# Kernel tuning notes

Measured on AMD Instinct MI355X. Metric: run time of the kernel, lower is better.

## Reference

```python
import jax, jax.numpy as jnp
from jax import lax
import numpy as np

B, T, H, W = 2, 16, 128, 128
HID = 256
EPS = 1e-5


def _conv(x, w):
    # x: (N,C,H,W), w: (O,I,3,3), stride 1, pad 1 ('SAME')
    return lax.conv_general_dilated(x, w, (1, 1), 'SAME',
                                    dimension_numbers=('NCHW', 'OIHW', 'NCHW'))


def _cnn_block(x, w, b, g, be, m, v):
    # conv -> BatchNorm (eval mode) -> ReLU -> MaxPool2d(2)
    y = _conv(x, w) + b[None, :, None, None]
    scale = (g * lax.rsqrt(v + EPS))[None, :, None, None]
    shift = (be - m * g * lax.rsqrt(v + EPS))[None, :, None, None]
    y = jax.nn.relu(y * scale + shift)
    return lax.reduce_window(y, -jnp.inf, lax.max,
                             (1, 1, 2, 2), (1, 1, 2, 2), 'VALID')


def _convlstm_layer(xs, Wg, bg):
    # xs: (T,B,Cin,h,w); gate conv on concat([x,h]) -> 4*HID channels
    _, nB, _, h, w = xs.shape
    h0 = jnp.zeros((nB, HID, h, w), xs.dtype)

    def step(carry, x_t):
        hprev, cprev = carry
        z = _conv(jnp.concatenate([x_t, hprev], axis=1), Wg) + bg[None, :, None, None]
        ci, cf, co, cg = jnp.split(z, 4, axis=1)
        c = jax.nn.sigmoid(cf) * cprev + jax.nn.sigmoid(ci) * jnp.tanh(cg)
        hn = jax.nn.sigmoid(co) * jnp.tanh(c)
        return (hn, c), hn

    (_, _), hs = lax.scan(step, (h0, h0), xs)
    return hs  # (T,B,HID,h,w)


def setup_inputs() -> dict:
    key = jax.random.key(0)
    ks = jax.random.split(key, 12)

    def rn(k, shape, s=0.05):
        return jax.random.normal(k, shape, jnp.float32) * s

    inp = {'x': jax.random.normal(ks[0], (B, T, 1, H, W), jnp.float32)}
    chans = [(1, 64), (64, 128), (128, 256)]
    for i, (ci, co) in enumerate(chans):
        inp[f'w{i}'] = rn(ks[1 + i], (co, ci, 3, 3))
        inp[f'b{i}'] = jnp.zeros((co,), jnp.float32)
        inp[f'g{i}'] = jnp.ones((co,), jnp.float32)
        inp[f'be{i}'] = jnp.zeros((co,), jnp.float32)
        inp[f'm{i}'] = rn(ks[4 + i], (co,), 0.01)
        inp[f'v{i}'] = jnp.ones((co,), jnp.float32)
    for l in range(2):
        cin = 256 if l == 0 else HID
        inp[f'lw{l}'] = rn(ks[7 + l], (4 * HID, cin + HID, 3, 3))
        inp[f'lb{l}'] = jnp.zeros((4 * HID,), jnp.float32)
    return inp


def reference(x, w0, b0, g0, be0, m0, v0,
              w1, b1, g1, be1, m1, v1,
              w2, b2, g2, be2, m2, v2,
              lw0, lb0, lw1, lb1):
    nB, nT = x.shape[0], x.shape[1]
    y = x.reshape(nB * nT, x.shape[2], x.shape[3], x.shape[4])
    y = _cnn_block(y, w0, b0, g0, be0, m0, v0)   # (BT,64,64,64)
    y = _cnn_block(y, w1, b1, g1, be1, m1, v1)   # (BT,128,32,32)
    y = _cnn_block(y, w2, b2, g2, be2, m2, v2)   # (BT,256,16,16)
    y = y.reshape(nB, nT, y.shape[1], y.shape[2], y.shape[3])
    xs = jnp.transpose(y, (1, 0, 2, 3, 4))       # (T,B,256,16,16)
    hs = _convlstm_layer(xs, lw0, lb0)
    hs = _convlstm_layer(hs, lw1, lb1)
    z_seq = jnp.transpose(hs, (1, 0, 2, 3, 4))   # (B,T,HID,16,16)
    z_last = z_seq[:, -1]
    return (z_seq, z_last)
```

## Files before the change

### kernel.cpp

```cpp
#include <hip/hip_runtime.h>
#include <hip/hip_bf16.h>
#include <cstddef>
#include <cstdint>

#define BN_EPS 1e-5f

typedef __attribute__((ext_vector_type(8))) _Float16 half8;
typedef __attribute__((ext_vector_type(4))) _Float16 half4;
typedef __attribute__((ext_vector_type(4))) float f32x4;

#define GLOBAL_AS __attribute__((address_space(1)))
#define LDS_AS    __attribute__((address_space(3)))

__device__ __forceinline__ void gload_lds16(const void* g, void* l) {
    __builtin_amdgcn_global_load_lds((const GLOBAL_AS uint32_t*)g,
                                     (LDS_AS uint32_t*)l, 16, 0, 0);
}

__device__ __forceinline__ float sigmoidf_(float x) {
    return 1.f / (1.f + __expf(-x));
}
__device__ __forceinline__ float tanhf_(float x) {
    float e = __expf(2.f * x);
    return 1.f - 2.f / (e + 1.f);
}

template <int CI, int OC, int S, int OCB>
__global__ __launch_bounds__(256) void cnn_block1_kernel(
    const float* __restrict__ in, const float* __restrict__ w,
    const float* __restrict__ bias, const float* __restrict__ g,
    const float* __restrict__ be, const float* __restrict__ m,
    const float* __restrict__ v, _Float16* __restrict__ out)
{
    constexpr int PS  = S / 2;
    constexpr int NQ  = (PS * PS) / 256;
    constexpr int NOG = OC / OCB;
    __shared__ float wl[OCB * CI * 9];

    int bid  = blockIdx.x;
    int quad = bid % NQ;
    int t2   = bid / NQ;
    int ocg  = t2 % NOG;
    int img  = t2 / NOG;
    int tid  = threadIdx.x;
    int oc0  = ocg * OCB;

    const float* wsrc = w + (size_t)oc0 * CI * 9;
    for (int i = tid; i < OCB * CI * 9; i += 256) wl[i] = wsrc[i];
    __syncthreads();

    int pp = quad * 256 + tid;
    int pr = pp / PS, pc = pp % PS;
    int r0 = 2 * pr - 1, c0 = 2 * pc - 1;

    int  roff[4], coff[4];
    bool rok[4], cok[4];
#pragma unroll
    for (int i = 0; i < 4; i++) {
        int rr = r0 + i; rok[i] = (rr >= 0 && rr < S); roff[i] = min(max(rr, 0), S - 1) * S;
        int cc = c0 + i; cok[i] = (cc >= 0 && cc < S); coff[i] = min(max(cc, 0), S - 1);
    }

    float acc[OCB][4];
#pragma unroll
    for (int o = 0; o < OCB; o++)
#pragma unroll
        for (int j = 0; j < 4; j++) acc[o][j] = 0.f;

    const float* ip = in + (size_t)img * CI * S * S;
    for (int ci = 0; ci < CI; ++ci) {
        float patch[4][4];
#pragma unroll
        for (int iy = 0; iy < 4; iy++)
#pragma unroll
            for (int ix = 0; ix < 4; ix++) {
                float val = ip[roff[iy] + coff[ix]];
                patch[iy][ix] = (rok[iy] && cok[ix]) ? val : 0.f;
            }
#pragma unroll
        for (int o = 0; o < OCB; o++) {
            const float* wp = wl + ((size_t)o * CI + ci) * 9;
#pragma unroll
            for (int ky = 0; ky < 3; ky++)
#pragma unroll
                for (int kx = 0; kx < 3; kx++) {
                    float ww = wp[ky * 3 + kx];
                    acc[o][0] += ww * patch[ky][kx];
                    acc[o][1] += ww * patch[ky][kx + 1];
                    acc[o][2] += ww * patch[ky + 1][kx];
                    acc[o][3] += ww * patch[ky + 1][kx + 1];
                }
        }
        ip += S * S;
    }

    half8 hv;
#pragma unroll
    for (int o = 0; o < OCB; o++) {
        int oc = oc0 + o;
        float scale = g[oc] * rsqrtf(v[oc] + BN_EPS);
        float shift = be[oc] - m[oc] * scale + bias[oc] * scale;
        float r00 = fmaxf(acc[o][0] * scale + shift, 0.f);
        float r01 = fmaxf(acc[o][1] * scale + shift, 0.f);
        float r10 = fmaxf(acc[o][2] * scale + shift, 0.f);
        float r11 = fmaxf(acc[o][3] * scale + shift, 0.f);
        hv[o] = (_Float16)fmaxf(fmaxf(r00, r01), fmaxf(r10, r11));
    }
    *(half8*)(&out[((size_t)img * (PS * PS) + pp) * OC + oc0]) = hv;
}

template <int OC, int CI>
__global__ __launch_bounds__(256) void wprep_conv_kernel(
    const float* __restrict__ W, _Float16* __restrict__ Wc)
{
    constexpr int K  = CI * 9;
    constexpr int CH = K / 8;
    int idx = blockIdx.x * 256 + threadIdx.x;
    if (idx >= OC * CH) return;
    int oc = idx / CH, chunk = idx % CH;
    int k0   = chunk * 8;
    int kcp  = (k0 >> 3) & 3;
    int kcl  = kcp ^ ((oc >> 1) & 3);
    int klog = (k0 & ~31) | (kcl << 3);
    int tap = klog / CI, ci = klog % CI;
    const float* src = W + ((size_t)oc * CI + ci) * 9 + tap;
    _Float16* dst = Wc + (size_t)oc * K + k0;
#pragma unroll
    for (int j = 0; j < 8; ++j) dst[j] = (_Float16)src[(size_t)j * 9];
}

__global__ __launch_bounds__(256) void wprep_kernel(
    const float* __restrict__ W, _Float16* __restrict__ Wp)
{
    int idx   = blockIdx.x * 256 + threadIdx.x;
    int row   = idx / 576;
    int chunk = idx % 576;
    int k0    = chunk * 8;
    int kcell = k0 >> 5;
    int kcp   = (k0 >> 3) & 3;
    int kcl   = kcp ^ ((row >> 1) & 3);
    int klog  = kcell * 32 + kcl * 8;
    int c = row >> 2, ggate = row & 3;
    int zc = ggate * 256 + c;
    int part = (klog >= 2304) ? 1 : 0;
    int rem  = klog - part * 2304;
    int tap  = rem >> 8;
    int ci   = rem & 255;
    const float* src = W + (size_t)zc * 4608 + (size_t)(part * 256 + ci) * 9 + tap;
    _Float16* dst = Wp + (size_t)row * 4608 + k0;
#pragma unroll
    for (int j = 0; j < 8; ++j) dst[j] = (_Float16)src[(size_t)j * 9];
}

template <int CI, int OC, int SIN>
__global__ __launch_bounds__(256) void conv_mfma_kernel(
    const _Float16* __restrict__ Wc, const _Float16* __restrict__ in,
    const float* __restrict__ bias, const float* __restrict__ g,
    const float* __restrict__ be, const float* __restrict__ m,
    const float* __restrict__ v, const _Float16* __restrict__ zpage,
    _Float16* __restrict__ out)
{
    constexpr int K    = CI * 9;
    constexpr int KS   = K / 32;
    constexpr int SPT  = CI / 32;
    constexpr int NPX  = SIN * SIN;
    constexpr int POOL = SIN / 2;
    constexpr int NPP  = NPX / 4;
    constexpr int NT     = (32 * NPX) / 64;
    constexpr int NCHUNK = NT / 8;

    __shared__ _Float16 Al[2][4096];
    __shared__ _Float16 Bl[2][2048];

    const int tid = threadIdx.x;
    const int gx   = blockIdx.x & 7;
    const int rest = blockIdx.x >> 3;
    const int nb   = gx * NCHUNK + (rest % NCHUNK);
    const int bm   = rest / NCHUNK;

    const int n0  = nb * 64;
    const int img = n0 / NPX;
    const int r   = n0 - img * NPX;

    const int srow = tid >> 2;
    const int kc   = tid & 3;
    const int kcs  = kc ^ ((srow >> 1) & 3);
    const int wid  = tid >> 6;

    const _Float16* aptr  = Wc + (size_t)(bm * 128 + srow) * K + kc * 8;
    const _Float16* aptr2 = aptr + (size_t)64 * K;

    const int rn   = r + srow;
    const int ppix = rn >> 2, quad = rn & 3;
    const int y = (ppix / POOL) * 2 + (quad >> 1);
    const int x = (ppix % POOL) * 2 + (quad & 1);
    const _Float16* imgbase = in + (size_t)img * NPX * CI;

    const int lane = tid & 63;
    const int kq   = lane >> 4;
    const int acol = lane & 15;
    int a_off[2], b_off[4];
#pragma unroll
    for (int mf = 0; mf < 2; mf++) {
        int arow = wid * 32 + mf * 16 + acol;
        a_off[mf] = arow * 64 + ((kq ^ ((arow >> 1) & 3)) << 4);
    }
#pragma unroll
    for (int nf = 0; nf < 4; nf++) {
        int brow = nf * 16 + acol;
        b_off[nf] = brow * 64 + ((kq ^ ((brow >> 1) & 3)) << 4);
    }

    f32x4 acc[2][4];
#pragma unroll
    for (int mf = 0; mf < 2; mf++)
#pragma unroll
        for (int nf = 0; nf < 4; nf++) acc[mf][nf] = {0.f, 0.f, 0.f, 0.f};

    auto stage = [&](int s, int buf) {
        gload_lds16(aptr  + (size_t)s * 32, (char*)&Al[buf][0] + wid * 1024);
        gload_lds16(aptr2 + (size_t)s * 32, (char*)&Al[buf][0] + 4096 + wid * 1024);
        int tap = s / SPT;
        int ci0 = (s % SPT) * 32;
        int dy = tap / 3 - 1, dx = tap - (tap / 3) * 3 - 1;
        int yy = y + dy, xx = x + dx;
        bool ok = (yy >= 0) && (yy < SIN) && (xx >= 0) && (xx < SIN);
        const _Float16* base = ok ? (imgbase + (size_t)(yy * SIN + xx) * CI) : zpage;
        gload_lds16(base + ci0 + kcs * 8, (char*)&Bl[buf][0] + wid * 1024);
    };

    stage(0, 0);
    __syncthreads();

    for (int s = 0; s < KS; ++s) {
        int cur = s & 1;
        if (s + 1 < KS) stage(s + 1, cur ^ 1);

        half8 af[2], bf[4];
#pragma unroll
        for (int mf = 0; mf < 2; mf++)
            af[mf] = *(const half8*)((const char*)&Al[cur][0] + a_off[mf]);
#pragma unroll
        for (int nf = 0; nf < 4; nf++)
            bf[nf] = *(const half8*)((const char*)&Bl[cur][0] + b_off[nf]);
#pragma unroll
        for (int mf = 0; mf < 2; mf++)
#pragma unroll
            for (int nf = 0; nf < 4; nf++)
                acc[mf][nf] = __builtin_amdgcn_mfma_f32_16x16x32_f16(
                    af[mf], bf[nf], acc[mf][nf], 0, 0, 0);

        __syncthreads();
    }

#pragma unroll
    for (int mf = 0; mf < 2; mf++) {
        const int oc0w = bm * 128 + wid * 32 + mf * 16 + kq * 4;
        float sc[4], sh[4];
#pragma unroll
        for (int j = 0; j < 4; j++) {
            int oc = oc0w + j;
            sc[j] = g[oc] * rsqrtf(v[oc] + BN_EPS);
            sh[j] = be[oc] - m[oc] * sc[j] + bias[oc] * sc[j];
        }
#pragma unroll
        for (int nf = 0; nf < 4; nf++) {
            f32x4 a = acc[mf][nf];
            half4 hv;
#pragma unroll
            for (int j = 0; j < 4; j++) {
                float val = fmaxf(a[j] * sc[j] + sh[j], 0.f);
                val = fmaxf(val, __shfl_xor(val, 1));
                val = fmaxf(val, __shfl_xor(val, 2));
                hv[j] = (_Float16)val;
            }
            if ((acol & 3) == 0) {
                int pl = (r + nf * 16 + acol) >> 2;
                *(half4*)(&out[((size_t)img * NPP + pl) * OC + oc0w]) = hv;
            }
        }
    }
}

struct Seg {
    const _Float16* W;
    const float* lbias;
    const _Float16* hsrc; long hs;
    _Float16* zx;  long zxs;
    float* cstate;
    _Float16* hdst; long hds;
    float* outseq; long osb;
    float* outlast;
    int mode;
};

__global__ __launch_bounds__(256, 4) void lstm3_kernel(
    Seg s0, Seg s1, Seg s2, Seg s3, int e0, int e1, int e2,
    const _Float16* __restrict__ zpage)
{
    __shared__ _Float16 Al[6][2048];
    __shared__ _Float16 Bl[6][1024];

    const int b = blockIdx.x;
    Seg S; int i;
    if (b < e0)      { S = s0; i = b; }
    else if (b < e1) { S = s1; i = b - e0; }
    else if (b < e2) { S = s2; i = b - e1; }
    else             { S = s3; i = b - e2; }

    const int tid = threadIdx.x;
    const int bm  = (i & 7) | (((i >> 3) & 1) << 3);
    const int nn  = i >> 4;
    const int img = nn >> 3;
    const int px0 = (nn & 7) * 32;

    const int wid  = tid >> 6;
    const int lane = tid & 63;
    const int lrow = lane >> 2;
    const int kc   = lane & 3;
    const int rowt = wid * 16 + lrow;
    const int kcs  = kc ^ ((rowt >> 1) & 3);

    const _Float16* aptr = S.W + (size_t)(bm * 64 + rowt) * 4608 + kc * 8;

    const int p_pix = px0 + rowt;
    const int py = p_pix >> 4, px = p_pix & 15;

    const _Float16* srcH = S.hsrc + (size_t)img * S.hs;

    const int kq   = lane >> 4;
    const int acol = lane & 15;
    const int arow = wid * 16 + acol;
    const int a_off  = arow * 64 + ((kq ^ ((arow >> 1) & 3)) << 4);
    const int b_off0 = acol * 64 + ((kq ^ ((acol >> 1) & 3)) << 4);
    const int brow1  = 16 + acol;
    const int b_off1 = brow1 * 64 + ((kq ^ ((brow1 >> 1) & 3)) << 4);

    f32x4 acc0 = {0.f, 0.f, 0.f, 0.f};
    f32x4 acc1 = {0.f, 0.f, 0.f, 0.f};

    const int NPAIR = 36;

    auto stage_pair = [&](int sp, int b2) {
        gload_lds16(aptr + (size_t)sp * 32,       (char*)&Al[b2][0]     + wid * 1024);
        gload_lds16(aptr + (size_t)(sp + 1) * 32, (char*)&Al[b2 + 1][0] + wid * 1024);
        if (wid < 2) {
            int tap = sp >> 3;
            int cc  = sp & 7;
            int t3  = tap / 3;
            int dy = t3 - 1, dx = tap - t3 * 3 - 1;
            int yy = py + dy, xx = px + dx;
            bool ok = (yy >= 0) && (yy < 16) && (xx >= 0) && (xx < 16);
            const _Float16* bsrc = ok ? (srcH + (size_t)(yy * 16 + xx) * 256) : zpage;
            const _Float16* p0 = bsrc + cc * 32 + kcs * 8;
            gload_lds16(p0,      (char*)&Bl[b2][0]     + wid * 1024);
            gload_lds16(p0 + 32, (char*)&Bl[b2 + 1][0] + wid * 1024);
        }
    };

    stage_pair(0, 0);
    stage_pair(2, 2);

    int cb = 0;
    int ib = 4;
    for (int p = 0; p < NPAIR; ++p) {
        __builtin_amdgcn_sched_barrier(0);
        if (wid < 2) {
            if (p < NPAIR - 1) asm volatile("s_waitcnt vmcnt(4)" ::: "memory");
            else               asm volatile("s_waitcnt vmcnt(0)" ::: "memory");
        } else {
            if (p < NPAIR - 1) asm volatile("s_waitcnt vmcnt(2)" ::: "memory");
            else               asm volatile("s_waitcnt vmcnt(0)" ::: "memory");
        }
        __builtin_amdgcn_s_barrier();
        int sp = 2 * p + 4;
        if (sp < 72) stage_pair(sp, ib);

        {
            half8 af  = *(const half8*)((const char*)&Al[cb][0] + a_off);
            half8 bf0 = *(const half8*)((const char*)&Bl[cb][0] + b_off0);
            half8 bf1 = *(const half8*)((const char*)&Bl[cb][0] + b_off1);
            acc0 = __builtin_amdgcn_mfma_f32_16x16x32_f16(af, bf0, acc0, 0, 0, 0);
            acc1 = __builtin_amdgcn_mfma_f32_16x16x32_f16(af, bf1, acc1, 0, 0, 0);
        }
        {
            half8 af  = *(const half8*)((const char*)&Al[cb + 1][0] + a_off);
            half8 bf0 = *(const half8*)((const char*)&Bl[cb + 1][0] + b_off0);
            half8 bf1 = *(const half8*)((const char*)&Bl[cb + 1][0] + b_off1);
            acc0 = __builtin_amdgcn_mfma_f32_16x16x32_f16(af, bf0, acc0, 0, 0, 0);
            acc1 = __builtin_amdgcn_mfma_f32_16x16x32_f16(af, bf1, acc1, 0, 0, 0);
        }

        cb = (cb == 4) ? 0 : cb + 2;
        ib = (ib == 4) ? 0 : ib + 2;
    }

    const int c = bm * 16 + wid * 4 + kq;

    if (S.mode == 1) {
#pragma unroll
        for (int cN = 0; cN < 2; ++cN) {
            f32x4 a = cN ? acc1 : acc0;
            int pxg = px0 + cN * 16 + acol;
            half4 hv;
#pragma unroll
            for (int j = 0; j < 4; j++) hv[j] = (_Float16)a[j];
            *(half4*)(&S.zx[(size_t)img * S.zxs + ((size_t)c * 256 + pxg) * 4]) = hv;
        }
        return;
    }

    float bi  = S.lbias[c];
    float bf_ = S.lbias[256 + c];
    float bo  = S.lbias[512 + c];
    float bg  = S.lbias[768 + c];

#pragma unroll
    for (int cN = 0; cN < 2; ++cN) {
        f32x4 a = cN ? acc1 : acc0;
        int pxg = px0 + cN * 16 + acol;
        half4 zv = *(const half4*)(&S.zx[(size_t)img * S.zxs + ((size_t)c * 256 + pxg) * 4]);
        size_t off = (size_t)img * 65536 + (size_t)c * 256 + pxg;
        float zi = a[0] + (float)zv[0] + bi;
        float zf = a[1] + (float)zv[1] + bf_;
        float zo = a[2] + (float)zv[2] + bo;
        float zg = a[3] + (float)zv[3] + bg;
        float cold = S.cstate[off];
        float cn = sigmoidf_(zf) * cold + sigmoidf_(zi) * tanhf_(zg);
        float hn = sigmoidf_(zo) * tanhf_(cn);
        S.cstate[off] = cn;
        S.hdst[(size_t)img * S.hds + (size_t)pxg * 256 + c] = (_Float16)hn;
        if (S.outseq) {
            S.outseq[(size_t)img * S.osb + (size_t)c * 256 + pxg] = hn;
            if (S.outlast)
                S.outlast[(size_t)img * 65536 + (size_t)c * 256 + pxg] = hn;
        }
    }
}

extern "C" void kernel_launch(void* const* d_in, const int* in_sizes, int n_in,
                              void* d_out, int out_size, void* d_ws, size_t ws_size,
                              hipStream_t stream)
{
    const float* x   = (const float*)d_in[0];
    const float* w0  = (const float*)d_in[1];
    const float* b0  = (const float*)d_in[2];
    const float* g0  = (const float*)d_in[3];
    const float* be0 = (const float*)d_in[4];
    const float* m0  = (const float*)d_in[5];
    const float* v0  = (const float*)d_in[6];
    const float* w1  = (const float*)d_in[7];
    const float* b1  = (const float*)d_in[8];
    const float* g1  = (const float*)d_in[9];
    const float* be1 = (const float*)d_in[10];
    const float* m1  = (const float*)d_in[11];
    const float* v1  = (const float*)d_in[12];
    const float* w2  = (const float*)d_in[13];
    const float* b2  = (const float*)d_in[14];
    const float* g2  = (const float*)d_in[15];
    const float* be2 = (const float*)d_in[16];
    const float* m2  = (const float*)d_in[17];
    const float* v2  = (const float*)d_in[18];
    const float* lw0 = (const float*)d_in[19];
    const float* lb0 = (const float*)d_in[20];
    const float* lw1 = (const float*)d_in[21];
    const float* lb1 = (const float*)d_in[22];

    float* out = (float*)d_out;

    char* base = (char*)d_ws;
    _Float16* Wp0  = (_Float16*)(base);
    _Float16* Wp1  = (_Float16*)(base + 9437184);
    _Float16* h0s  = (_Float16*)(base + 18874368);
    _Float16* y2h  = (_Float16*)(base + 25165824);
    _Float16* Wc2  = (_Float16*)(base + 29360128);
    _Float16* Wc3  = (_Float16*)(base + 29507584);
    _Float16* zpg  = (_Float16*)(base + 30097408);
    _Float16* hb1a = (_Float16*)(base + 30228480);
    _Float16* hb1b = (_Float16*)(base + 30490624);
    float*    cst0 = (float*)(base + 30752768);
    float*    cst1 = (float*)(base + 31277056);
    _Float16* zx1a = (_Float16*)(base + 31801344);
    _Float16* zx1b = (_Float16*)(base + 32849920);
    _Float16* zx0  = (_Float16*)(base + 33898496);
    _Float16* y0   = (_Float16*)(base);
    _Float16* y1   = (_Float16*)(base + 16777216);

    hipMemsetAsync(zpg, 0, 131072, stream);

    cnn_block1_kernel<1, 64, 128, 8><<<32 * 8 * 16, 256, 0, stream>>>(
        x, w0, b0, g0, be0, m0, v0, y0);
    wprep_conv_kernel<128, 64><<<36, 256, 0, stream>>>(w1, Wc2);
    conv_mfma_kernel<64, 128, 64><<<2048, 256, 0, stream>>>(
        Wc2, y0, b1, g1, be1, m1, v1, zpg, y1);
    wprep_conv_kernel<256, 128><<<144, 256, 0, stream>>>(w2, Wc3);
    conv_mfma_kernel<128, 256, 32><<<1024, 256, 0, stream>>>(
        Wc3, y1, b2, g2, be2, m2, v2, zpg, y2h);

    wprep_kernel<<<2304, 256, 0, stream>>>(lw0, Wp0);
    wprep_kernel<<<2304, 256, 0, stream>>>(lw1, Wp1);

    hipMemsetAsync(cst0, 0, (size_t)2 * 524288, stream);

    const long IS = 16 * 65536;

    auto makeD = [&](int t) {
        Seg D{};
        D.W = Wp0; D.lbias = lb0;
        D.hsrc = y2h + (size_t)t * 65536; D.hs = IS;
        D.zx = zx0 + (size_t)t * 262144; D.zxs = 16 * 262144;
        D.cstate = nullptr; D.hdst = nullptr; D.hds = 0;
        D.outseq = nullptr; D.osb = 0; D.outlast = nullptr; D.mode = 1;
        return D;
    };

    {
        Seg D0 = makeD(0), D1 = makeD(1);
        lstm3_kernel<<<512, 256, 0, stream>>>(D0, D1, D1, D1, 256, 512, 512, zpg);
    }

    for (int d = 0; d <= 17; ++d) {
        const bool doA = (d <= 15);
        const bool doC = (d >= 1 && d <= 16);
        const bool doB = (d >= 2);
        const bool doD = (d <= 13);

        Seg segs[4]; int ns = 0; int cum = 0; int ends[4];
        if (doA) {
            int t = d;
            Seg A{};
            A.W = Wp0 + 2304; A.lbias = lb0;
            A.hsrc = (t == 0) ? zpg : (h0s + (size_t)(t - 1) * 65536);
            A.hs   = (t == 0) ? 0 : IS;
            A.zx = zx0 + (size_t)t * 262144; A.zxs = 16 * 262144;
            A.cstate = cst0;
            A.hdst = h0s + (size_t)t * 65536; A.hds = IS;
            A.outseq = nullptr; A.osb = 0; A.outlast = nullptr; A.mode = 0;
            segs[ns] = A; cum += 256; ends[ns++] = cum;
        }
        if (doC) {
            int u = d - 1;
            Seg C{};
            C.W = Wp1; C.lbias = lb1;
            C.hsrc = h0s + (size_t)u * 65536; C.hs = IS;
            C.zx = (u & 1) ? zx1b : zx1a; C.zxs = 262144;
            C.cstate = nullptr; C.hdst = nullptr; C.hds = 0;
            C.outseq = nullptr; C.osb = 0; C.outlast = nullptr; C.mode = 1;
            segs[ns] = C; cum += 256; ends[ns++] = cum;
        }
        if (doB) {
            int v = d - 2;
            Seg B{};
            B.W = Wp1 + 2304; B.lbias = lb1;
            B.hsrc = (v == 0) ? zpg : ((v & 1) ? hb1a : hb1b);
            B.hs   = (v == 0) ? 0 : 65536;
            B.zx = (v & 1) ? zx1b : zx1a; B.zxs = 262144;
            B.cstate = cst1;
            B.hdst = (v & 1) ? hb1b : hb1a; B.hds = 65536;
            B.outseq = out + (size_t)v * 65536; B.osb = 1048576;
            B.outlast = (v == 15) ? (out + 2097152) : nullptr; B.mode = 0;
            segs[ns] = B; cum += 256; ends[ns++] = cum;
        }
        if (doD) {
            segs[ns] = makeD(d + 2); cum += 256; ends[ns++] = cum;
        }
        for (int k = ns; k < 4; ++k) segs[k] = segs[0];
        int e0 = ends[0];
        int e1 = (ns > 1) ? ends[1] : cum;
        int e2 = (ns > 2) ? ends[2] : cum;
        lstm3_kernel<<<cum, 256, 0, stream>>>(
            segs[0], segs[1], segs[2], segs[3], e0, e1, e2, zpg);
    }
}
```

Measured before the change: 572.8 us.

## Deepen conv pipeline to triple-buffered pairs and widen LSTM pixel tiles

The CNN conv kernel moves from a double-buffered single-step K loop with full __syncthreads to a triple-buffered pair-staged pipeline with explicit vmcnt waits, prefetching two K-steps ahead. The ConvLSTM kernel doubles its pixel tile from 32 to 64 per block, so each A-tile load feeds four MFMAs instead of two and all waves stage B. This halves the grid size per segment. The goal is better latency hiding and weight reuse, at the cost of more LDS per block and lower occupancy (launch bounds 2), plus fewer blocks in flight for the latency-bound recurrent steps.

```diff
diff --git a/kernel.cpp b/kernel.cpp
--- a/kernel.cpp
+++ b/kernel.cpp
@@ -153,7 +153,7 @@
 }
 
 template <int CI, int OC, int SIN>
-__global__ __launch_bounds__(256) void conv_mfma_kernel(
+__global__ __launch_bounds__(256, 2) void conv_mfma_kernel(
     const _Float16* __restrict__ Wc, const _Float16* __restrict__ in,
     const float* __restrict__ bias, const float* __restrict__ g,
     const float* __restrict__ be, const float* __restrict__ m,
@@ -162,6 +162,7 @@
 {
     constexpr int K    = CI * 9;
     constexpr int KS   = K / 32;
+    constexpr int NP   = KS / 2;
     constexpr int SPT  = CI / 32;
     constexpr int NPX  = SIN * SIN;
     constexpr int POOL = SIN / 2;
@@ -169,8 +170,8 @@
     constexpr int NT     = (32 * NPX) / 64;
     constexpr int NCHUNK = NT / 8;
 
-    __shared__ _Float16 Al[2][4096];
-    __shared__ _Float16 Bl[2][2048];
+    __shared__ _Float16 Al[6][4096];
+    __shared__ _Float16 Bl[6][2048];
 
     const int tid = threadIdx.x;
     const int gx   = blockIdx.x & 7;
@@ -217,40 +218,54 @@
 #pragma unroll
         for (int nf = 0; nf < 4; nf++) acc[mf][nf] = {0.f, 0.f, 0.f, 0.f};
 
-    auto stage = [&](int s, int buf) {
-        gload_lds16(aptr  + (size_t)s * 32, (char*)&Al[buf][0] + wid * 1024);
-        gload_lds16(aptr2 + (size_t)s * 32, (char*)&Al[buf][0] + 4096 + wid * 1024);
-        int tap = s / SPT;
-        int ci0 = (s % SPT) * 32;
+    auto stage_pair = [&](int sp, int b2) {
+        gload_lds16(aptr  + (size_t)sp * 32,       (char*)&Al[b2][0]            + wid * 1024);
+        gload_lds16(aptr  + (size_t)(sp + 1) * 32, (char*)&Al[b2 + 1][0]        + wid * 1024);
+        gload_lds16(aptr2 + (size_t)sp * 32,       (char*)&Al[b2][0]     + 4096 + wid * 1024);
+        gload_lds16(aptr2 + (size_t)(sp + 1) * 32, (char*)&Al[b2 + 1][0] + 4096 + wid * 1024);
+        int tap = sp / SPT;
+        int ci0 = (sp % SPT) * 32;
         int dy = tap / 3 - 1, dx = tap - (tap / 3) * 3 - 1;
         int yy = y + dy, xx = x + dx;
         bool ok = (yy >= 0) && (yy < SIN) && (xx >= 0) && (xx < SIN);
         const _Float16* base = ok ? (imgbase + (size_t)(yy * SIN + xx) * CI) : zpage;
-        gload_lds16(base + ci0 + kcs * 8, (char*)&Bl[buf][0] + wid * 1024);
+        const _Float16* p0 = base + ci0 + kcs * 8;
+        gload_lds16(p0,      (char*)&Bl[b2][0]     + wid * 1024);
+        gload_lds16(p0 + 32, (char*)&Bl[b2 + 1][0] + wid * 1024);
     };
 
-    stage(0, 0);
-    __syncthreads();
-
-    for (int s = 0; s < KS; ++s) {
-        int cur = s & 1;
-        if (s + 1 < KS) stage(s + 1, cur ^ 1);
-
-        half8 af[2], bf[4];
-#pragma unroll
-        for (int mf = 0; mf < 2; mf++)
-            af[mf] = *(const half8*)((const char*)&Al[cur][0] + a_off[mf]);
-#pragma unroll
-        for (int nf = 0; nf < 4; nf++)
-            bf[nf] = *(const half8*)((const char*)&Bl[cur][0] + b_off[nf]);
-#pragma unroll
-        for (int mf = 0; mf < 2; mf++)
+    stage_pair(0, 0);
+    stage_pair(2, 2);
+
+    int cb = 0, ib = 4;
+    for (int p = 0; p < NP; ++p) {
+        __builtin_amdgcn_sched_barrier(0);
+        if (p < NP - 1) asm volatile("s_waitcnt vmcnt(6)" ::: "memory");
+        else            asm volatile("s_waitcnt vmcnt(0)" ::: "memory");
+        __builtin_amdgcn_s_barrier();
+        int sp = 2 * p + 4;
+        if (sp < KS) stage_pair(sp, ib);
+
+#pragma unroll
+        for (int hs = 0; hs < 2; ++hs) {
+            const int bb = cb + hs;
+            half8 af[2], bf[4];
+#pragma unroll
+            for (int mf = 0; mf < 2; mf++)
+                af[mf] = *(const half8*)((const char*)&Al[bb][0] + a_off[mf]);
 #pragma unroll
             for (int nf = 0; nf < 4; nf++)
-                acc[mf][nf] = __builtin_amdgcn_mfma_f32_16x16x32_f16(
-                    af[mf], bf[nf], acc[mf][nf], 0, 0, 0);
-
-        __syncthreads();
+                bf[nf] = *(const half8*)((const char*)&Bl[bb][0] + b_off[nf]);
+#pragma unroll
+            for (int mf = 0; mf < 2; mf++)
+#pragma unroll
+                for (int nf = 0; nf < 4; nf++)
+                    acc[mf][nf] = __builtin_amdgcn_mfma_f32_16x16x32_f16(
+                        af[mf], bf[nf], acc[mf][nf], 0, 0, 0);
+        }
+
+        cb = (cb == 4) ? 0 : cb + 2;
+        ib = (ib == 4) ? 0 : ib + 2;
     }
 
 #pragma unroll
@@ -294,12 +309,12 @@
     int mode;
 };
 
-__global__ __launch_bounds__(256, 4) void lstm3_kernel(
+__global__ __launch_bounds__(256, 2) void lstm3_kernel(
     Seg s0, Seg s1, Seg s2, Seg s3, int e0, int e1, int e2,
     const _Float16* __restrict__ zpage)
 {
     __shared__ _Float16 Al[6][2048];
-    __shared__ _Float16 Bl[6][1024];
+    __shared__ _Float16 Bl[6][2048];
 
     const int b = blockIdx.x;
     Seg S; int i;
@@ -310,9 +325,9 @@
 
     const int tid = threadIdx.x;
     const int bm  = (i & 7) | (((i >> 3) & 1) << 3);
-    const int nn  = i >> 4;
-    const int img = nn >> 3;
-    const int px0 = (nn & 7) * 32;
+    const int nb  = i >> 4;
+    const int img = nb >> 2;
+    const int px0 = (nb & 3) * 64;
 
     const int wid  = tid >> 6;
     const int lane = tid & 63;
@@ -331,64 +346,56 @@
     const int kq   = lane >> 4;
     const int acol = lane & 15;
     const int arow = wid * 16 + acol;
-    const int a_off  = arow * 64 + ((kq ^ ((arow >> 1) & 3)) << 4);
-    const int b_off0 = acol * 64 + ((kq ^ ((acol >> 1) & 3)) << 4);
-    const int brow1  = 16 + acol;
-    const int b_off1 = brow1 * 64 + ((kq ^ ((brow1 >> 1) & 3)) << 4);
-
-    f32x4 acc0 = {0.f, 0.f, 0.f, 0.f};
-    f32x4 acc1 = {0.f, 0.f, 0.f, 0.f};
+    const int a_off = arow * 64 + ((kq ^ ((arow >> 1) & 3)) << 4);
+    int b_off[4];
+#pragma unroll
+    for (int nf = 0; nf < 4; nf++) {
+        int brow = nf * 16 + acol;
+        b_off[nf] = brow * 64 + ((kq ^ ((brow >> 1) & 3)) << 4);
+    }
+
+    f32x4 acc[4];
+#pragma unroll
+    for (int nf = 0; nf < 4; nf++) acc[nf] = {0.f, 0.f, 0.f, 0.f};
 
     const int NPAIR = 36;
 
     auto stage_pair = [&](int sp, int b2) {
         gload_lds16(aptr + (size_t)sp * 32,       (char*)&Al[b2][0]     + wid * 1024);
         gload_lds16(aptr + (size_t)(sp + 1) * 32, (char*)&Al[b2 + 1][0] + wid * 1024);
-        if (wid < 2) {
-            int tap = sp >> 3;
-            int cc  = sp & 7;
-            int t3  = tap / 3;
-            int dy = t3 - 1, dx = tap - t3 * 3 - 1;
-            int yy = py + dy, xx = px + dx;
-            bool ok = (yy >= 0) && (yy < 16) && (xx >= 0) && (xx < 16);
-            const _Float16* bsrc = ok ? (srcH + (size_t)(yy * 16 + xx) * 256) : zpage;
-            const _Float16* p0 = bsrc + cc * 32 + kcs * 8;
-            gload_lds16(p0,      (char*)&Bl[b2][0]     + wid * 1024);
-            gload_lds16(p0 + 32, (char*)&Bl[b2 + 1][0] + wid * 1024);
-        }
+        int tap = sp >> 3;
+        int cc  = sp & 7;
+        int t3  = tap / 3;
+        int dy = t3 - 1, dx = tap - t3 * 3 - 1;
+        int yy = py + dy, xx = px + dx;
+        bool ok = (yy >= 0) && (yy < 16) && (xx >= 0) && (xx < 16);
+        const _Float16* bsrc = ok ? (srcH + (size_t)(yy * 16 + xx) * 256) : zpage;
+        const _Float16* p0 = bsrc + cc * 32 + kcs * 8;
+        gload_lds16(p0,      (char*)&Bl[b2][0]     + wid * 1024);
+        gload_lds16(p0 + 32, (char*)&Bl[b2 + 1][0] + wid * 1024);
     };
 
     stage_pair(0, 0);
     stage_pair(2, 2);
 
-    int cb = 0;
-    int ib = 4;
+    int cb = 0, ib = 4;
     for (int p = 0; p < NPAIR; ++p) {
         __builtin_amdgcn_sched_barrier(0);
-        if (wid < 2) {
-            if (p < NPAIR - 1) asm volatile("s_waitcnt vmcnt(4)" ::: "memory");
-            else               asm volatile("s_waitcnt vmcnt(0)" ::: "memory");
-        } else {
-            if (p < NPAIR - 1) asm volatile("s_waitcnt vmcnt(2)" ::: "memory");
-            else               asm volatile("s_waitcnt vmcnt(0)" ::: "memory");
-        }
+        if (p < NPAIR - 1) asm volatile("s_waitcnt vmcnt(4)" ::: "memory");
+        else               asm volatile("s_waitcnt vmcnt(0)" ::: "memory");
         __builtin_amdgcn_s_barrier();
         int sp = 2 * p + 4;
         if (sp < 72) stage_pair(sp, ib);
 
-        {
-            half8 af  = *(const half8*)((const char*)&Al[cb][0] + a_off);
-            half8 bf0 = *(const half8*)((const char*)&Bl[cb][0] + b_off0);
-            half8 bf1 = *(const half8*)((const char*)&Bl[cb][0] + b_off1);
-            acc0 = __builtin_amdgcn_mfma_f32_16x16x32_f16(af, bf0, acc0, 0, 0, 0);
-            acc1 = __builtin_amdgcn_mfma_f32_16x16x32_f16(af, bf1, acc1, 0, 0, 0);
-        }
-        {
-            half8 af  = *(const half8*)((const char*)&Al[cb + 1][0] + a_off);
-            half8 bf0 = *(const half8*)((const char*)&Bl[cb + 1][0] + b_off0);
-            half8 bf1 = *(const half8*)((const char*)&Bl[cb + 1][0] + b_off1);
-            acc0 = __builtin_amdgcn_mfma_f32_16x16x32_f16(af, bf0, acc0, 0, 0, 0);
-            acc1 = __builtin_amdgcn_mfma_f32_16x16x32_f16(af, bf1, acc1, 0, 0, 0);
+#pragma unroll
+        for (int hs = 0; hs < 2; ++hs) {
+            const int bb = cb + hs;
+            half8 af = *(const half8*)((const char*)&Al[bb][0] + a_off);
+#pragma unroll
+            for (int nf = 0; nf < 4; nf++) {
+                half8 bf = *(const half8*)((const char*)&Bl[bb][0] + b_off[nf]);
+                acc[nf] = __builtin_amdgcn_mfma_f32_16x16x32_f16(af, bf, acc[nf], 0, 0, 0);
+            }
         }
 
         cb = (cb == 4) ? 0 : cb + 2;
@@ -399,9 +406,9 @@
 
     if (S.mode == 1) {
 #pragma unroll
-        for (int cN = 0; cN < 2; ++cN) {
-            f32x4 a = cN ? acc1 : acc0;
-            int pxg = px0 + cN * 16 + acol;
+        for (int nf = 0; nf < 4; nf++) {
+            f32x4 a = acc[nf];
+            int pxg = px0 + nf * 16 + acol;
             half4 hv;
 #pragma unroll
             for (int j = 0; j < 4; j++) hv[j] = (_Float16)a[j];
@@ -416,9 +423,9 @@
     float bg  = S.lbias[768 + c];
 
 #pragma unroll
-    for (int cN = 0; cN < 2; ++cN) {
-        f32x4 a = cN ? acc1 : acc0;
-        int pxg = px0 + cN * 16 + acol;
+    for (int nf = 0; nf < 4; nf++) {
+        f32x4 a = acc[nf];
+        int pxg = px0 + nf * 16 + acol;
         half4 zv = *(const half4*)(&S.zx[(size_t)img * S.zxs + ((size_t)c * 256 + pxg) * 4]);
         size_t off = (size_t)img * 65536 + (size_t)c * 256 + pxg;
         float zi = a[0] + (float)zv[0] + bi;
@@ -516,7 +523,7 @@
 
     {
         Seg D0 = makeD(0), D1 = makeD(1);
-        lstm3_kernel<<<512, 256, 0, stream>>>(D0, D1, D1, D1, 256, 512, 512, zpg);
+        lstm3_kernel<<<256, 256, 0, stream>>>(D0, D1, D1, D1, 128, 256, 256, zpg);
     }
 
     for (int d = 0; d <= 17; ++d) {
@@ -536,7 +543,7 @@
             A.cstate = cst0;
             A.hdst = h0s + (size_t)t * 65536; A.hds = IS;
             A.outseq = nullptr; A.osb = 0; A.outlast = nullptr; A.mode = 0;
-            segs[ns] = A; cum += 256; ends[ns++] = cum;
+            segs[ns] = A; cum += 128; ends[ns++] = cum;
         }
         if (doC) {
             int u = d - 1;
@@ -546,7 +553,7 @@
             C.zx = (u & 1) ? zx1b : zx1a; C.zxs = 262144;
             C.cstate = nullptr; C.hdst = nullptr; C.hds = 0;
             C.outseq = nullptr; C.osb = 0; C.outlast = nullptr; C.mode = 1;
-            segs[ns] = C; cum += 256; ends[ns++] = cum;
+            segs[ns] = C; cum += 128; ends[ns++] = cum;
         }
         if (doB) {
             int v = d - 2;
@@ -559,10 +566,10 @@
             B.hdst = (v & 1) ? hb1b : hb1a; B.hds = 65536;
             B.outseq = out + (size_t)v * 65536; B.osb = 1048576;
             B.outlast = (v == 15) ? (out + 2097152) : nullptr; B.mode = 0;
-            segs[ns] = B; cum += 256; ends[ns++] = cum;
+            segs[ns] = B; cum += 128; ends[ns++] = cum;
         }
         if (doD) {
-            segs[ns] = makeD(d + 2); cum += 256; ends[ns++] = cum;
+            segs[ns] = makeD(d + 2); cum += 128; ends[ns++] = cum;
         }
         for (int k = ns; k < 4; ++k) segs[k] = segs[0];
         int e0 = ends[0];
```

Measured after the change: 618.8 us. +8.0%, slower.

## Deepen conv MFMA pipeline to triple-buffered pairs of K-steps with vmcnt waits

Applied to the files above, without the earlier changes.

Replaces the double-buffered one-K-step-per-iteration loop in the CNN conv kernel with a 6-slot LDS ring that loads two K-steps per stage and keeps two pairs in flight. It waits with explicit s_waitcnt vmcnt counts and one barrier per pair, which halves the barriers and hides more global-load latency. It also adds a launch_bounds occupancy hint of 2. LDS use triples to 72KB per block, which may limit occupancy. The code assumes KS is even and large enough for the prologue.

```diff
diff --git a/kernel.cpp b/kernel.cpp
--- a/kernel.cpp
+++ b/kernel.cpp
@@ -153,7 +153,7 @@
 }
 
 template <int CI, int OC, int SIN>
-__global__ __launch_bounds__(256) void conv_mfma_kernel(
+__global__ __launch_bounds__(256, 2) void conv_mfma_kernel(
     const _Float16* __restrict__ Wc, const _Float16* __restrict__ in,
     const float* __restrict__ bias, const float* __restrict__ g,
     const float* __restrict__ be, const float* __restrict__ m,
@@ -162,6 +162,7 @@
 {
     constexpr int K    = CI * 9;
     constexpr int KS   = K / 32;
+    constexpr int NP   = KS / 2;
     constexpr int SPT  = CI / 32;
     constexpr int NPX  = SIN * SIN;
     constexpr int POOL = SIN / 2;
@@ -169,8 +170,8 @@
     constexpr int NT     = (32 * NPX) / 64;
     constexpr int NCHUNK = NT / 8;
 
-    __shared__ _Float16 Al[2][4096];
-    __shared__ _Float16 Bl[2][2048];
+    __shared__ _Float16 Al[6][4096];
+    __shared__ _Float16 Bl[6][2048];
 
     const int tid = threadIdx.x;
     const int gx   = blockIdx.x & 7;
@@ -217,40 +218,54 @@
 #pragma unroll
         for (int nf = 0; nf < 4; nf++) acc[mf][nf] = {0.f, 0.f, 0.f, 0.f};
 
-    auto stage = [&](int s, int buf) {
-        gload_lds16(aptr  + (size_t)s * 32, (char*)&Al[buf][0] + wid * 1024);
-        gload_lds16(aptr2 + (size_t)s * 32, (char*)&Al[buf][0] + 4096 + wid * 1024);
-        int tap = s / SPT;
-        int ci0 = (s % SPT) * 32;
+    auto stage_pair = [&](int sp, int b2) {
+        gload_lds16(aptr  + (size_t)sp * 32,       (char*)&Al[b2][0]            + wid * 1024);
+        gload_lds16(aptr  + (size_t)(sp + 1) * 32, (char*)&Al[b2 + 1][0]        + wid * 1024);
+        gload_lds16(aptr2 + (size_t)sp * 32,       (char*)&Al[b2][0]     + 4096 + wid * 1024);
+        gload_lds16(aptr2 + (size_t)(sp + 1) * 32, (char*)&Al[b2 + 1][0] + 4096 + wid * 1024);
+        int tap = sp / SPT;
+        int ci0 = (sp % SPT) * 32;
         int dy = tap / 3 - 1, dx = tap - (tap / 3) * 3 - 1;
         int yy = y + dy, xx = x + dx;
         bool ok = (yy >= 0) && (yy < SIN) && (xx >= 0) && (xx < SIN);
         const _Float16* base = ok ? (imgbase + (size_t)(yy * SIN + xx) * CI) : zpage;
-        gload_lds16(base + ci0 + kcs * 8, (char*)&Bl[buf][0] + wid * 1024);
+        const _Float16* p0 = base + ci0 + kcs * 8;
+        gload_lds16(p0,      (char*)&Bl[b2][0]     + wid * 1024);
+        gload_lds16(p0 + 32, (char*)&Bl[b2 + 1][0] + wid * 1024);
     };
 
-    stage(0, 0);
-    __syncthreads();
-
-    for (int s = 0; s < KS; ++s) {
-        int cur = s & 1;
-        if (s + 1 < KS) stage(s + 1, cur ^ 1);
-
-        half8 af[2], bf[4];
-#pragma unroll
-        for (int mf = 0; mf < 2; mf++)
-            af[mf] = *(const half8*)((const char*)&Al[cur][0] + a_off[mf]);
-#pragma unroll
-        for (int nf = 0; nf < 4; nf++)
-            bf[nf] = *(const half8*)((const char*)&Bl[cur][0] + b_off[nf]);
-#pragma unroll
-        for (int mf = 0; mf < 2; mf++)
+    stage_pair(0, 0);
+    stage_pair(2, 2);
+
+    int cb = 0, ib = 4;
+    for (int p = 0; p < NP; ++p) {
+        __builtin_amdgcn_sched_barrier(0);
+        if (p < NP - 1) asm volatile("s_waitcnt vmcnt(6)" ::: "memory");
+        else            asm volatile("s_waitcnt vmcnt(0)" ::: "memory");
+        __builtin_amdgcn_s_barrier();
+        int sp = 2 * p + 4;
+        if (sp < KS) stage_pair(sp, ib);
+
+#pragma unroll
+        for (int hs = 0; hs < 2; ++hs) {
+            const int bb = cb + hs;
+            half8 af[2], bf[4];
+#pragma unroll
+            for (int mf = 0; mf < 2; mf++)
+                af[mf] = *(const half8*)((const char*)&Al[bb][0] + a_off[mf]);
 #pragma unroll
             for (int nf = 0; nf < 4; nf++)
-                acc[mf][nf] = __builtin_amdgcn_mfma_f32_16x16x32_f16(
-                    af[mf], bf[nf], acc[mf][nf], 0, 0, 0);
-
-        __syncthreads();
+                bf[nf] = *(const half8*)((const char*)&Bl[bb][0] + b_off[nf]);
+#pragma unroll
+            for (int mf = 0; mf < 2; mf++)
+#pragma unroll
+                for (int nf = 0; nf < 4; nf++)
+                    acc[mf][nf] = __builtin_amdgcn_mfma_f32_16x16x32_f16(
+                        af[mf], bf[nf], acc[mf][nf], 0, 0, 0);
+        }
+
+        cb = (cb == 4) ? 0 : cb + 2;
+        ib = (ib == 4) ? 0 : ib + 2;
     }
 
 #pragma unroll
```

Result: no change. 573.9 us (+0.2%).
